# Optimization experiments

Measured on AMD Instinct MI355X. Metric: run time of the kernel, lower is better.

Reference implementation:

```python
import jax, jax.numpy as jnp
import numpy as np

N_NODES = 50000
N_EDGES = 800000
VOCAB = 100000
EMB = 64
HID = 64
N_CLASSES = 10
N_GRAPHS = 512


def setup_inputs() -> dict:
    key = jax.random.key(0)
    ks = jax.random.split(key, 12)
    node_ids = jax.random.randint(ks[0], (N_NODES,), 0, VOCAB)
    edge_index = jax.random.randint(ks[1], (2, N_EDGES), 0, N_NODES)
    batch = jnp.sort(jax.random.randint(ks[2], (N_NODES,), 0, N_GRAPHS))
    emb = jax.random.normal(ks[3], (VOCAB, EMB), jnp.float32)
    s_e = 1.0 / np.sqrt(EMB)
    s_h = 1.0 / np.sqrt(HID)
    Wl0 = jax.random.normal(ks[4], (EMB, HID), jnp.float32) * s_e
    bl0 = jnp.zeros((HID,), jnp.float32)
    Wr0 = jax.random.normal(ks[5], (EMB, HID), jnp.float32) * s_e
    Wl1 = jax.random.normal(ks[6], (HID, HID), jnp.float32) * s_h
    bl1 = jnp.zeros((HID,), jnp.float32)
    Wr1 = jax.random.normal(ks[7], (HID, HID), jnp.float32) * s_h
    Wout = jax.random.normal(ks[8], (HID, N_CLASSES), jnp.float32) * s_h
    bout = jnp.zeros((N_CLASSES,), jnp.float32)
    return {"node_ids": node_ids, "edge_index": edge_index, "batch": batch,
            "emb": emb, "Wl0": Wl0, "bl0": bl0, "Wr0": Wr0,
            "Wl1": Wl1, "bl1": bl1, "Wr1": Wr1, "Wout": Wout, "bout": bout}


def _sage_conv(x, src, dst, Wl, bl, Wr):
    # PyG SAGEConv (aggr='mean'): out_i = lin_l(mean_{j in N(i)} x_j) + lin_r(x_i)
    msg = x[src]                                      # [E, d] gather
    s = jax.ops.segment_sum(msg, dst, num_segments=N_NODES)
    cnt = jax.ops.segment_sum(jnp.ones((msg.shape[0], 1), x.dtype), dst,
                              num_segments=N_NODES)
    mean = jnp.where(cnt > 0, s / jnp.maximum(cnt, 1), 0)
    return mean @ Wl + bl + x @ Wr


def reference(node_ids, edge_index, batch, emb, Wl0, bl0, Wr0, Wl1, bl1, Wr1, Wout, bout):
    x = emb[node_ids]                                  # [N, EMB]
    src, dst = edge_index[0], edge_index[1]
    x = jax.nn.relu(_sage_conv(x, src, dst, Wl0, bl0, Wr0))
    x = jax.nn.relu(_sage_conv(x, src, dst, Wl1, bl1, Wr1))
    # global_mean_pool over graph ids
    s = jax.ops.segment_sum(x, batch, num_segments=N_GRAPHS)
    cnt = jax.ops.segment_sum(jnp.ones((x.shape[0], 1), x.dtype), batch,
                              num_segments=N_GRAPHS)
    pooled = jnp.where(cnt > 0, s / jnp.maximum(cnt, 1), 0)   # [G, HID]
    return pooled @ Wout + bout                        # [G, N_CLASSES]
```

## Files before the change

kernel.cpp:

```cpp
#include <hip/hip_runtime.h>
#include <hip/hip_bf16.h>

#define N_NODES 50000
#define N_EDGES 800000
#define EMB 64
#define HID 64
#define N_CLASSES 10
#define N_GRAPHS 512

#define BKT_SHIFT 6
#define BKT_NODES 64
#define NB_BKT ((N_NODES + BKT_NODES - 1) / BKT_NODES)
#define BKT_CAP 1408
#define CNT_STRIDE 16
#define EB_CHUNK 4096
#define EB_PER_THR (EB_CHUNK / 256)
#define EB_BLOCKS ((N_EDGES + EB_CHUNK - 1) / EB_CHUNK)
#define XFORM_BLOCKS ((N_NODES + 63) / 64)
#define XPAD 68

#define ACC8(vv, A)                                                            \
    do {                                                                       \
        A[0] += __uint_as_float((vv).x << 16);                                 \
        A[1] += __uint_as_float((vv).x & 0xFFFF0000u);                         \
        A[2] += __uint_as_float((vv).y << 16);                                 \
        A[3] += __uint_as_float((vv).y & 0xFFFF0000u);                         \
        A[4] += __uint_as_float((vv).z << 16);                                 \
        A[5] += __uint_as_float((vv).z & 0xFFFF0000u);                         \
        A[6] += __uint_as_float((vv).w << 16);                                 \
        A[7] += __uint_as_float((vv).w & 0xFFFF0000u);                         \
    } while (0)

__device__ __forceinline__ void build_local_csr(
    int bucket, const int* __restrict__ cnt, const int* __restrict__ ebuf,
    unsigned short* lcsr, int* nhist, int* sval, int* sexcl, int* ncur) {
    int tid = threadIdx.x;
    int bs = bucket * BKT_CAP;
    int ne = min(cnt[bucket * CNT_STRIDE], BKT_CAP);
    if (tid < BKT_NODES) { nhist[tid] = 0; ncur[tid] = 0; }
    __syncthreads();
    int held[6];
    int nh = 0;
    for (int i = tid; i < ne; i += 256) held[nh++] = ebuf[bs + i];
#pragma unroll
    for (int j = 0; j < 6; j++)
        if (j < nh) atomicAdd(&nhist[held[j] >> 16], 1);
    __syncthreads();
    if (tid < 64) {
        int v = nhist[tid];
        int s = v;
#pragma unroll
        for (int off = 1; off < 64; off <<= 1) {
            int u = __shfl_up(s, off, 64);
            if (tid >= off) s += u;
        }
        sval[tid] = v;
        sexcl[tid] = s - v;
    }
    __syncthreads();
#pragma unroll
    for (int j = 0; j < 6; j++)
        if (j < nh) {
            int p = held[j];
            int l = p >> 16;
            int r = atomicAdd(&ncur[l], 1);
            lcsr[sexcl[l] + r] = (unsigned short)(p & 0xFFFF);
        }
    __syncthreads();
}

__device__ __forceinline__ void agg2(
    int sA, int dA, int sB, int dB, int sl,
    const unsigned short* lcsr, const __hip_bfloat16* __restrict__ Pb,
    float oA[8], float oB[8]) {
    float a0[8], a1[8], b0[8], b1[8];
#pragma unroll
    for (int j = 0; j < 8; j++) { a0[j] = 0.f; a1[j] = 0.f; b0[j] = 0.f; b1[j] = 0.f; }
    int eA = sA + dA, eB = sB + dB;
    int pA = sA, pB = sB;
    while ((pA + 8 <= eA) && (pB + 8 <= eB)) {
        uint4 vA[8], vB[8];
#pragma unroll
        for (int j = 0; j < 8; j++)
            vA[j] = ((const uint4*)(Pb + (size_t)lcsr[pA + j] * 64))[sl];
#pragma unroll
        for (int j = 0; j < 8; j++)
            vB[j] = ((const uint4*)(Pb + (size_t)lcsr[pB + j] * 64))[sl];
#pragma unroll
        for (int j = 0; j < 8; j++) ACC8(vA[j], ((j & 1) ? a1 : a0));
#pragma unroll
        for (int j = 0; j < 8; j++) ACC8(vB[j], ((j & 1) ? b1 : b0));
        pA += 8; pB += 8;
    }
    while (pA + 8 <= eA) {
        uint4 v[8];
#pragma unroll
        for (int j = 0; j < 8; j++)
            v[j] = ((const uint4*)(Pb + (size_t)lcsr[pA + j] * 64))[sl];
#pragma unroll
        for (int j = 0; j < 8; j++) ACC8(v[j], ((j & 1) ? a1 : a0));
        pA += 8;
    }
    while (pB + 8 <= eB) {
        uint4 v[8];
#pragma unroll
        for (int j = 0; j < 8; j++)
            v[j] = ((const uint4*)(Pb + (size_t)lcsr[pB + j] * 64))[sl];
#pragma unroll
        for (int j = 0; j < 8; j++) ACC8(v[j], ((j & 1) ? b1 : b0));
        pB += 8;
    }
    for (; pA < eA; ++pA) {
        uint4 v = ((const uint4*)(Pb + (size_t)lcsr[pA] * 64))[sl];
        ACC8(v, a0);
    }
    for (; pB < eB; ++pB) {
        uint4 v = ((const uint4*)(Pb + (size_t)lcsr[pB] * 64))[sl];
        ACC8(v, b0);
    }
    float invA = (dA > 0) ? 1.0f / (float)dA : 0.0f;
    float invB = (dB > 0) ? 1.0f / (float)dB : 0.0f;
#pragma unroll
    for (int j = 0; j < 8; j++) {
        oA[j] = (a0[j] + a1[j]) * invA;
        oB[j] = (b0[j] + b1[j]) * invB;
    }
}

__device__ __forceinline__ void finish_row(int node, int sl,
                                           const float* __restrict__ H,
                                           float m[8], float* dst) {
    if (node < N_NODES) {
        size_t off = (size_t)node * 64 + sl * 8;
        float4 q0 = *(const float4*)&H[off];
        float4 q1 = *(const float4*)&H[off + 4];
        m[0] = fmaxf(m[0] + q0.x, 0.f);
        m[1] = fmaxf(m[1] + q0.y, 0.f);
        m[2] = fmaxf(m[2] + q0.z, 0.f);
        m[3] = fmaxf(m[3] + q0.w, 0.f);
        m[4] = fmaxf(m[4] + q1.x, 0.f);
        m[5] = fmaxf(m[5] + q1.y, 0.f);
        m[6] = fmaxf(m[6] + q1.z, 0.f);
        m[7] = fmaxf(m[7] + q1.w, 0.f);
    } else {
#pragma unroll
        for (int j = 0; j < 8; j++) m[j] = 0.f;
    }
    *(float4*)&dst[sl * 8] = make_float4(m[0], m[1], m[2], m[3]);
    *(float4*)&dst[sl * 8 + 4] = make_float4(m[4], m[5], m[6], m[7]);
}

__global__ __launch_bounds__(256) void k_combo(
    const int* __restrict__ esrc, const int* __restrict__ edst,
    int* __restrict__ cnt, int* __restrict__ ebuf,
    const int* __restrict__ ids, const float* __restrict__ emb,
    const float* __restrict__ Wl, const float* __restrict__ bl,
    const float* __restrict__ Wr,
    __hip_bfloat16* __restrict__ Pb, float* __restrict__ Qout) {
    __shared__ float sW[64 * 64];
    __shared__ float sX[64 * XPAD];
    int t = threadIdx.x;
    if (blockIdx.x < EB_BLOCKS) {
        int* h = (int*)sW;
        int* bbase = h + NB_BKT;
        int* cur = (int*)sX;
        for (int i = t; i < NB_BKT; i += 256) { h[i] = 0; cur[i] = 0; }
        __syncthreads();
        int base = blockIdx.x * EB_CHUNK;
        int end = min(base + EB_CHUNK, N_EDGES);
        int dreg[EB_PER_THR];
        int nd = 0;
        for (int i = base + t; i < end; i += 256) dreg[nd++] = edst[i];
#pragma unroll
        for (int j = 0; j < EB_PER_THR; j++)
            if (j < nd) atomicAdd(&h[dreg[j] >> BKT_SHIFT], 1);
        __syncthreads();
        for (int i = t; i < NB_BKT; i += 256)
            if (h[i]) bbase[i] = i * BKT_CAP + atomicAdd(&cnt[i * CNT_STRIDE], h[i]);
        __syncthreads();
        {
            int j = 0;
            for (int i = base + t; i < end; i += 256, j++) {
                int d = dreg[j], s = esrc[i];
                int b = d >> BKT_SHIFT;
                int r = atomicAdd(&cur[b], 1);
                int slot = bbase[b] + r;
                if (slot < (b + 1) * BKT_CAP)
                    ebuf[slot] = ((d & (BKT_NODES - 1)) << 16) | s;
            }
        }
        return;
    }
    int tile = (blockIdx.x - EB_BLOCKS) * 64;
    for (int i = t; i < 64 * 16; i += 256)
        ((float4*)sW)[i] = ((const float4*)Wl)[i];
    for (int i = t; i < 64 * 16; i += 256) {
        int r = i >> 4, c = i & 15;
        int node = tile + r;
        float4 v = make_float4(0.f, 0.f, 0.f, 0.f);
        if (node < N_NODES)
            v = ((const float4*)(emb + (size_t)ids[node] * 64))[c];
        *(float4*)&sX[r * XPAD + c * 4] = v;
    }
    __syncthreads();
    int dg = t & 15, ng = t >> 4;
    float acc[4][4];
#pragma unroll
    for (int i = 0; i < 4; i++)
#pragma unroll
        for (int j = 0; j < 4; j++) acc[i][j] = 0.f;
#pragma unroll 4
    for (int k = 0; k < 64; k++) {
        float4 w = *(const float4*)&sW[k * 64 + dg * 4];
#pragma unroll
        for (int i = 0; i < 4; i++) {
            float xv = sX[(ng + i * 16) * XPAD + k];
            acc[i][0] = fmaf(xv, w.x, acc[i][0]);
            acc[i][1] = fmaf(xv, w.y, acc[i][1]);
            acc[i][2] = fmaf(xv, w.z, acc[i][2]);
            acc[i][3] = fmaf(xv, w.w, acc[i][3]);
        }
    }
#pragma unroll
    for (int i = 0; i < 4; i++) {
        int node = tile + ng + i * 16;
        if (node < N_NODES) {
            union { ushort4 u; __hip_bfloat16 h[4]; } pk;
            pk.h[0] = __float2bfloat16(acc[i][0]);
            pk.h[1] = __float2bfloat16(acc[i][1]);
            pk.h[2] = __float2bfloat16(acc[i][2]);
            pk.h[3] = __float2bfloat16(acc[i][3]);
            *(ushort4*)&Pb[(size_t)node * 64 + dg * 4] = pk.u;
        }
    }
    __syncthreads();
    for (int i = t; i < 64 * 16; i += 256)
        ((float4*)sW)[i] = ((const float4*)Wr)[i];
    __syncthreads();
#pragma unroll
    for (int i = 0; i < 4; i++)
#pragma unroll
        for (int j = 0; j < 4; j++) acc[i][j] = 0.f;
#pragma unroll 4
    for (int k = 0; k < 64; k++) {
        float4 w = *(const float4*)&sW[k * 64 + dg * 4];
#pragma unroll
        for (int i = 0; i < 4; i++) {
            float xv = sX[(ng + i * 16) * XPAD + k];
            acc[i][0] = fmaf(xv, w.x, acc[i][0]);
            acc[i][1] = fmaf(xv, w.y, acc[i][1]);
            acc[i][2] = fmaf(xv, w.z, acc[i][2]);
            acc[i][3] = fmaf(xv, w.w, acc[i][3]);
        }
    }
    float4 blv = *(const float4*)&bl[dg * 4];
#pragma unroll
    for (int i = 0; i < 4; i++) {
        int node = tile + ng + i * 16;
        if (node < N_NODES)
            *(float4*)&Qout[(size_t)node * 64 + dg * 4] =
                make_float4(acc[i][0] + blv.x, acc[i][1] + blv.y,
                            acc[i][2] + blv.z, acc[i][3] + blv.w);
    }
}

__global__ __launch_bounds__(256, 4) void k_fused1(
    const int* __restrict__ cnt, const int* __restrict__ ebuf,
    const __hip_bfloat16* __restrict__ Pb0, const float* __restrict__ Wl,
    const float* __restrict__ bl, const float* __restrict__ Wr,
    __hip_bfloat16* __restrict__ Pb1, float* __restrict__ H) {
    __shared__ float sW[64 * 64];
    __shared__ float sX[64 * XPAD];
    __shared__ unsigned short lcsr[BKT_CAP];
    __shared__ int nhist[BKT_NODES], sval[BKT_NODES], sexcl[BKT_NODES], ncur[BKT_NODES];
    int t = threadIdx.x;
    int tile = blockIdx.x * 64;
    for (int i = t; i < 64 * 16; i += 256)
        ((float4*)sW)[i] = ((const float4*)Wl)[i];
    build_local_csr(blockIdx.x, cnt, ebuf, lcsr, nhist, sval, sexcl, ncur);
    int grp = t >> 3, sl = t & 7;
    int ln0 = grp * 2, ln1 = ln0 + 1;
    float mA[8], mB[8];
    agg2(sexcl[ln0], sval[ln0], sexcl[ln1], sval[ln1], sl, lcsr, Pb0, mA, mB);
    finish_row(tile + ln0, sl, H, mA, &sX[ln0 * XPAD]);
    finish_row(tile + ln1, sl, H, mB, &sX[ln1 * XPAD]);
    __syncthreads();
    int dg = t & 15, ng = t >> 4;
    float acc[4][4];
#pragma unroll
    for (int i = 0; i < 4; i++)
#pragma unroll
        for (int j = 0; j < 4; j++) acc[i][j] = 0.f;
#pragma unroll 4
    for (int k = 0; k < 64; k++) {
        float4 w = *(const float4*)&sW[k * 64 + dg * 4];
#pragma unroll
        for (int i = 0; i < 4; i++) {
            float xv = sX[(ng + i * 16) * XPAD + k];
            acc[i][0] = fmaf(xv, w.x, acc[i][0]);
            acc[i][1] = fmaf(xv, w.y, acc[i][1]);
            acc[i][2] = fmaf(xv, w.z, acc[i][2]);
            acc[i][3] = fmaf(xv, w.w, acc[i][3]);
        }
    }
#pragma unroll
    for (int i = 0; i < 4; i++) {
        int node = tile + ng + i * 16;
        if (node < N_NODES) {
            union { ushort4 u; __hip_bfloat16 h[4]; } pk;
            pk.h[0] = __float2bfloat16(acc[i][0]);
            pk.h[1] = __float2bfloat16(acc[i][1]);
            pk.h[2] = __float2bfloat16(acc[i][2]);
            pk.h[3] = __float2bfloat16(acc[i][3]);
            *(ushort4*)&Pb1[(size_t)node * 64 + dg * 4] = pk.u;
        }
    }
    __syncthreads();
    for (int i = t; i < 64 * 16; i += 256)
        ((float4*)sW)[i] = ((const float4*)Wr)[i];
    __syncthreads();
#pragma unroll
    for (int i = 0; i < 4; i++)
#pragma unroll
        for (int j = 0; j < 4; j++) acc[i][j] = 0.f;
#pragma unroll 4
    for (int k = 0; k < 64; k++) {
        float4 w = *(const float4*)&sW[k * 64 + dg * 4];
#pragma unroll
        for (int i = 0; i < 4; i++) {
            float xv = sX[(ng + i * 16) * XPAD + k];
            acc[i][0] = fmaf(xv, w.x, acc[i][0]);
            acc[i][1] = fmaf(xv, w.y, acc[i][1]);
            acc[i][2] = fmaf(xv, w.z, acc[i][2]);
            acc[i][3] = fmaf(xv, w.w, acc[i][3]);
        }
    }
    float4 blv = *(const float4*)&bl[dg * 4];
#pragma unroll
    for (int i = 0; i < 4; i++) {
        int node = tile + ng + i * 16;
        if (node < N_NODES)
            *(float4*)&H[(size_t)node * 64 + dg * 4] =
                make_float4(acc[i][0] + blv.x, acc[i][1] + blv.y,
                            acc[i][2] + blv.z, acc[i][3] + blv.w);
    }
}

__global__ __launch_bounds__(256, 4) void k_agg2_pool(
    const int* __restrict__ cnt, const int* __restrict__ ebuf,
    const __hip_bfloat16* __restrict__ Pb, const float* __restrict__ H,
    const int* __restrict__ batch, float* __restrict__ psum) {
    __shared__ float sPool[64 * 64];
    __shared__ unsigned short lcsr[BKT_CAP];
    __shared__ int nhist[BKT_NODES], sval[BKT_NODES], sexcl[BKT_NODES], ncur[BKT_NODES];
    __shared__ int sLg[64];
    int t = threadIdx.x;
    int nb = blockIdx.x * 64;
    int gmin = batch[nb];
    if (t < 64) {
        int node = nb + t;
        sLg[t] = batch[node < N_NODES ? node : (N_NODES - 1)] - gmin;
    }
    build_local_csr(blockIdx.x, cnt, ebuf, lcsr, nhist, sval, sexcl, ncur);
    int grp = t >> 3, sl = t & 7;
    int ln0 = grp * 2, ln1 = ln0 + 1;
    float mA[8], mB[8];
    agg2(sexcl[ln0], sval[ln0], sexcl[ln1], sval[ln1], sl, lcsr, Pb, mA, mB);
    finish_row(nb + ln0, sl, H, mA, &sPool[ln0 * 64]);
    finish_row(nb + ln1, sl, H, mB, &sPool[ln1 * 64]);
    __syncthreads();
    int d = t & 63, q = t >> 6;
    int n0 = q * 16;
    float run = 0.f;
    int cur = sLg[n0];
    for (int n = n0; n < n0 + 16; n++) {
        int lg = sLg[n];
        if (lg != cur) {
            if (run != 0.f)
                atomicAdd(&psum[(size_t)(gmin + cur) * 64 + d], run);
            run = 0.f;
            cur = lg;
        }
        run += sPool[n * 64 + d];
    }
    if (run != 0.f)
        atomicAdd(&psum[(size_t)(gmin + cur) * 64 + d], run);
}

__device__ __forceinline__ int lower_bound_batch(const int* __restrict__ batch, int val) {
    int lo = 0, hi = N_NODES;
    while (lo < hi) {
        int mid = (lo + hi) >> 1;
        if (batch[mid] < val) lo = mid + 1; else hi = mid;
    }
    return lo;
}

__global__ __launch_bounds__(256) void k_out(
    const int* __restrict__ batch, const float* __restrict__ psum,
    const float* __restrict__ Wout, const float* __restrict__ bout,
    float* __restrict__ out) {
    int w = threadIdx.x >> 6, lane = threadIdx.x & 63;
    int g = blockIdx.x * 4 + w;
    if (g >= N_GRAPHS) return;
    int s0 = lower_bound_batch(batch, g);
    int s1 = lower_bound_batch(batch, g + 1);
    int cntg = s1 - s0;
    float inv = (cntg > 0) ? 1.0f / (float)cntg : 0.0f;
    float pooled = psum[(size_t)g * 64 + lane] * inv;
#pragma unroll
    for (int c = 0; c < N_CLASSES; c++) {
        float v = pooled * Wout[lane * N_CLASSES + c];
#pragma unroll
        for (int off = 32; off > 0; off >>= 1) v += __shfl_down(v, off, 64);
        if (lane == 0) out[(size_t)g * N_CLASSES + c] = v + bout[c];
    }
}


extern "C" void kernel_launch(void* const* d_in, const int* in_sizes, int n_in,
                              void* d_out, int out_size, void* d_ws, size_t ws_size,
                              hipStream_t stream) {
    const int*   node_ids = (const int*)d_in[0];
    const int*   edge_idx = (const int*)d_in[1];
    const int*   batch    = (const int*)d_in[2];
    const float* emb      = (const float*)d_in[3];
    const float* Wl0      = (const float*)d_in[4];
    const float* bl0      = (const float*)d_in[5];
    const float* Wr0      = (const float*)d_in[6];
    const float* Wl1      = (const float*)d_in[7];
    const float* bl1      = (const float*)d_in[8];
    const float* Wr1      = (const float*)d_in[9];
    const float* Wout     = (const float*)d_in[10];
    const float* bout     = (const float*)d_in[11];
    float* out = (float*)d_out;

    const int* esrc = edge_idx;
    const int* edst = edge_idx + N_EDGES;

    __hip_bfloat16* Pb0 = (__hip_bfloat16*)d_ws;
    __hip_bfloat16* Pb1 = Pb0 + (size_t)N_NODES * 64;
    float* H = (float*)(Pb1 + (size_t)N_NODES * 64);
    int* ebuf = (int*)(H + (size_t)N_NODES * 64);
    int* cnt = ebuf + (size_t)NB_BKT * BKT_CAP;
    float* psum = (float*)(cnt + (size_t)NB_BKT * CNT_STRIDE);

    const int BLK = 256;

    hipMemsetAsync(cnt, 0, (NB_BKT * CNT_STRIDE + N_GRAPHS * 64) * sizeof(int), stream);

    k_combo<<<EB_BLOCKS + XFORM_BLOCKS, BLK, 0, stream>>>(
        esrc, edst, cnt, ebuf, node_ids, emb, Wl0, bl0, Wr0, Pb0, H);

    k_fused1<<<XFORM_BLOCKS, BLK, 0, stream>>>(cnt, ebuf, Pb0, Wl1, bl1, Wr1, Pb1, H);

    k_agg2_pool<<<NB_BKT, BLK, 0, stream>>>(cnt, ebuf, Pb1, H, batch, psum);

    k_out<<<(N_GRAPHS + 3) / 4, BLK, 0, stream>>>(batch, psum, Wout, bout, out);
}
```

Before: 188.3 us.

## Pad CSR segments to a zero row, software-pipeline gathers, fuse dual GEMM

Pads each node's local CSR segment to a multiple of 8 entries, filling the padding with a dedicated all-zero sentinel row in the bf16 feature tables. This lets the aggregation loop issue fixed groups of 4 gathers, double-buffered across iterations, with no scalar tail loops. The two per-tile GEMMs (lin_l and lin_r) are merged into one pass that reads weights directly from global or L1 instead of staging them in shared memory. This frees LDS and removes barriers, but adds wasted gathers of the zero row and more accumulator registers.

Result: faster. 183.7 us (-2.5%).

```diff
diff --git a/kernel.cpp b/kernel.cpp
--- a/kernel.cpp
+++ b/kernel.cpp
@@ -18,6 +18,9 @@
 #define EB_BLOCKS ((N_EDGES + EB_CHUNK - 1) / EB_CHUNK)
 #define XFORM_BLOCKS ((N_NODES + 63) / 64)
 #define XPAD 68
+#define ZROW N_NODES
+#define LCSR_SZ 1856
+#define LCSR_FULL 1864
 
 #define ACC8(vv, A)                                                            \
     do {                                                                       \
@@ -38,6 +41,7 @@
     int bs = bucket * BKT_CAP;
     int ne = min(cnt[bucket * CNT_STRIDE], BKT_CAP);
     if (tid < BKT_NODES) { nhist[tid] = 0; ncur[tid] = 0; }
+    for (int i = tid; i < LCSR_FULL; i += 256) lcsr[i] = (unsigned short)ZROW;
     __syncthreads();
     int held[6];
     int nh = 0;
@@ -48,14 +52,15 @@
     __syncthreads();
     if (tid < 64) {
         int v = nhist[tid];
-        int s = v;
+        int p = (v + 7) & ~7;
+        int s = p;
 #pragma unroll
         for (int off = 1; off < 64; off <<= 1) {
             int u = __shfl_up(s, off, 64);
             if (tid >= off) s += u;
         }
         sval[tid] = v;
-        sexcl[tid] = s - v;
+        sexcl[tid] = s - p;
     }
     __syncthreads();
 #pragma unroll
@@ -76,47 +81,43 @@
     float a0[8], a1[8], b0[8], b1[8];
 #pragma unroll
     for (int j = 0; j < 8; j++) { a0[j] = 0.f; a1[j] = 0.f; b0[j] = 0.f; b1[j] = 0.f; }
-    int eA = sA + dA, eB = sB + dB;
-    int pA = sA, pB = sB;
-    while ((pA + 8 <= eA) && (pB + 8 <= eB)) {
-        uint4 vA[8], vB[8];
-#pragma unroll
-        for (int j = 0; j < 8; j++)
-            vA[j] = ((const uint4*)(Pb + (size_t)lcsr[pA + j] * 64))[sl];
-#pragma unroll
-        for (int j = 0; j < 8; j++)
-            vB[j] = ((const uint4*)(Pb + (size_t)lcsr[pB + j] * 64))[sl];
-#pragma unroll
-        for (int j = 0; j < 8; j++) ACC8(vA[j], ((j & 1) ? a1 : a0));
-#pragma unroll
-        for (int j = 0; j < 8; j++) ACC8(vB[j], ((j & 1) ? b1 : b0));
-        pA += 8; pB += 8;
-    }
-    while (pA + 8 <= eA) {
-        uint4 v[8];
-#pragma unroll
-        for (int j = 0; j < 8; j++)
-            v[j] = ((const uint4*)(Pb + (size_t)lcsr[pA + j] * 64))[sl];
-#pragma unroll
-        for (int j = 0; j < 8; j++) ACC8(v[j], ((j & 1) ? a1 : a0));
-        pA += 8;
-    }
-    while (pB + 8 <= eB) {
-        uint4 v[8];
-#pragma unroll
-        for (int j = 0; j < 8; j++)
-            v[j] = ((const uint4*)(Pb + (size_t)lcsr[pB + j] * 64))[sl];
-#pragma unroll
-        for (int j = 0; j < 8; j++) ACC8(v[j], ((j & 1) ? b1 : b0));
-        pB += 8;
-    }
-    for (; pA < eA; ++pA) {
-        uint4 v = ((const uint4*)(Pb + (size_t)lcsr[pA] * 64))[sl];
-        ACC8(v, a0);
-    }
-    for (; pB < eB; ++pB) {
-        uint4 v = ((const uint4*)(Pb + (size_t)lcsr[pB] * 64))[sl];
-        ACC8(v, b0);
+    int nA = (dA + 3) >> 2, nB = (dB + 3) >> 2;
+    int n = max(nA, nB);
+    int mA = max(nA - 1, 0), mB = max(nB - 1, 0);
+    if (n > 0) {
+        uint4 A0[4], A1[4], B0[4], B1[4];
+#define LD4(D, base_)                                                          \
+        {                                                                      \
+            int _p = (base_);                                                  \
+            D[0] = ((const uint4*)(Pb + (size_t)lcsr[_p + 0] * 64))[sl];       \
+            D[1] = ((const uint4*)(Pb + (size_t)lcsr[_p + 1] * 64))[sl];       \
+            D[2] = ((const uint4*)(Pb + (size_t)lcsr[_p + 2] * 64))[sl];       \
+            D[3] = ((const uint4*)(Pb + (size_t)lcsr[_p + 3] * 64))[sl];       \
+        }
+#define AC4(S, X0, X1)                                                         \
+        { ACC8(S[0], X0); ACC8(S[1], X1); ACC8(S[2], X0); ACC8(S[3], X1); }
+        LD4(A0, sA); LD4(B0, sB);
+        int c = 1;
+        for (; c + 1 < n; c += 2) {
+            LD4(A1, sA + 4 * min(c, mA)); LD4(B1, sB + 4 * min(c, mB));
+            if (c - 1 < nA) AC4(A0, a0, a1);
+            if (c - 1 < nB) AC4(B0, b0, b1);
+            LD4(A0, sA + 4 * min(c + 1, mA)); LD4(B0, sB + 4 * min(c + 1, mB));
+            if (c < nA) AC4(A1, a0, a1);
+            if (c < nB) AC4(B1, b0, b1);
+        }
+        if (c < n) {
+            LD4(A1, sA + 4 * min(c, mA)); LD4(B1, sB + 4 * min(c, mB));
+            if (c - 1 < nA) AC4(A0, a0, a1);
+            if (c - 1 < nB) AC4(B0, b0, b1);
+            if (c < nA) AC4(A1, a0, a1);
+            if (c < nB) AC4(B1, b0, b1);
+        } else {
+            if (c - 1 < nA) AC4(A0, a0, a1);
+            if (c - 1 < nB) AC4(B0, b0, b1);
+        }
+#undef LD4
+#undef AC4
     }
     float invA = (dA > 0) ? 1.0f / (float)dA : 0.0f;
     float invB = (dB > 0) ? 1.0f / (float)dB : 0.0f;
@@ -150,20 +151,71 @@
     *(float4*)&dst[sl * 8 + 4] = make_float4(m[4], m[5], m[6], m[7]);
 }
 
+__device__ __forceinline__ void gemm_dual_from_sX(
+    int tile, int t, const float* sX,
+    const float* __restrict__ Wl, const float* __restrict__ Wr,
+    const float* __restrict__ bl,
+    __hip_bfloat16* __restrict__ Pb, float* __restrict__ Qout) {
+    int dg = t & 15, ng = t >> 4;
+    float accL[4][4], accR[4][4];
+#pragma unroll
+    for (int i = 0; i < 4; i++)
+#pragma unroll
+        for (int j = 0; j < 4; j++) { accL[i][j] = 0.f; accR[i][j] = 0.f; }
+#pragma unroll 4
+    for (int k = 0; k < 64; k++) {
+        float4 wl = ((const float4*)Wl)[k * 16 + dg];
+        float4 wr = ((const float4*)Wr)[k * 16 + dg];
+#pragma unroll
+        for (int i = 0; i < 4; i++) {
+            float xv = sX[(ng + i * 16) * XPAD + k];
+            accL[i][0] = fmaf(xv, wl.x, accL[i][0]);
+            accL[i][1] = fmaf(xv, wl.y, accL[i][1]);
+            accL[i][2] = fmaf(xv, wl.z, accL[i][2]);
+            accL[i][3] = fmaf(xv, wl.w, accL[i][3]);
+            accR[i][0] = fmaf(xv, wr.x, accR[i][0]);
+            accR[i][1] = fmaf(xv, wr.y, accR[i][1]);
+            accR[i][2] = fmaf(xv, wr.z, accR[i][2]);
+            accR[i][3] = fmaf(xv, wr.w, accR[i][3]);
+        }
+    }
+    float4 blv = ((const float4*)bl)[dg];
+#pragma unroll
+    for (int i = 0; i < 4; i++) {
+        int node = tile + ng + i * 16;
+        if (node < N_NODES) {
+            union { ushort4 u; __hip_bfloat16 h[4]; } pk;
+            pk.h[0] = __float2bfloat16(accL[i][0]);
+            pk.h[1] = __float2bfloat16(accL[i][1]);
+            pk.h[2] = __float2bfloat16(accL[i][2]);
+            pk.h[3] = __float2bfloat16(accL[i][3]);
+            *(ushort4*)&Pb[(size_t)node * 64 + dg * 4] = pk.u;
+            *(float4*)&Qout[(size_t)node * 64 + dg * 4] =
+                make_float4(accR[i][0] + blv.x, accR[i][1] + blv.y,
+                            accR[i][2] + blv.z, accR[i][3] + blv.w);
+        }
+    }
+}
+
 __global__ __launch_bounds__(256) void k_combo(
     const int* __restrict__ esrc, const int* __restrict__ edst,
     int* __restrict__ cnt, int* __restrict__ ebuf,
     const int* __restrict__ ids, const float* __restrict__ emb,
     const float* __restrict__ Wl, const float* __restrict__ bl,
     const float* __restrict__ Wr,
-    __hip_bfloat16* __restrict__ Pb, float* __restrict__ Qout) {
-    __shared__ float sW[64 * 64];
+    __hip_bfloat16* __restrict__ Pb, __hip_bfloat16* __restrict__ Pb1z,
+    float* __restrict__ Qout) {
     __shared__ float sX[64 * XPAD];
     int t = threadIdx.x;
     if (blockIdx.x < EB_BLOCKS) {
-        int* h = (int*)sW;
+        if (blockIdx.x == 0 && t < 16) {
+            uint4 z = make_uint4(0u, 0u, 0u, 0u);
+            if (t < 8) ((uint4*)(Pb + (size_t)ZROW * 64))[t] = z;
+            else       ((uint4*)(Pb1z + (size_t)ZROW * 64))[t - 8] = z;
+        }
+        int* h = (int*)sX;
         int* bbase = h + NB_BKT;
-        int* cur = (int*)sX;
+        int* cur = bbase + NB_BKT;
         for (int i = t; i < NB_BKT; i += 256) { h[i] = 0; cur[i] = 0; }
         __syncthreads();
         int base = blockIdx.x * EB_CHUNK;
@@ -192,8 +244,6 @@
         return;
     }
     int tile = (blockIdx.x - EB_BLOCKS) * 64;
-    for (int i = t; i < 64 * 16; i += 256)
-        ((float4*)sW)[i] = ((const float4*)Wl)[i];
     for (int i = t; i < 64 * 16; i += 256) {
         int r = i >> 4, c = i & 15;
         int node = tile + r;
@@ -203,65 +253,7 @@
         *(float4*)&sX[r * XPAD + c * 4] = v;
     }
     __syncthreads();
-    int dg = t & 15, ng = t >> 4;
-    float acc[4][4];
-#pragma unroll
-    for (int i = 0; i < 4; i++)
-#pragma unroll
-        for (int j = 0; j < 4; j++) acc[i][j] = 0.f;
-#pragma unroll 4
-    for (int k = 0; k < 64; k++) {
-        float4 w = *(const float4*)&sW[k * 64 + dg * 4];
-#pragma unroll
-        for (int i = 0; i < 4; i++) {
-            float xv = sX[(ng + i * 16) * XPAD + k];
-            acc[i][0] = fmaf(xv, w.x, acc[i][0]);
-            acc[i][1] = fmaf(xv, w.y, acc[i][1]);
-            acc[i][2] = fmaf(xv, w.z, acc[i][2]);
-            acc[i][3] = fmaf(xv, w.w, acc[i][3]);
-        }
-    }
-#pragma unroll
-    for (int i = 0; i < 4; i++) {
-        int node = tile + ng + i * 16;
-        if (node < N_NODES) {
-            union { ushort4 u; __hip_bfloat16 h[4]; } pk;
-            pk.h[0] = __float2bfloat16(acc[i][0]);
-            pk.h[1] = __float2bfloat16(acc[i][1]);
-            pk.h[2] = __float2bfloat16(acc[i][2]);
-            pk.h[3] = __float2bfloat16(acc[i][3]);
-            *(ushort4*)&Pb[(size_t)node * 64 + dg * 4] = pk.u;
-        }
-    }
-    __syncthreads();
-    for (int i = t; i < 64 * 16; i += 256)
-        ((float4*)sW)[i] = ((const float4*)Wr)[i];
-    __syncthreads();
-#pragma unroll
-    for (int i = 0; i < 4; i++)
-#pragma unroll
-        for (int j = 0; j < 4; j++) acc[i][j] = 0.f;
-#pragma unroll 4
-    for (int k = 0; k < 64; k++) {
-        float4 w = *(const float4*)&sW[k * 64 + dg * 4];
-#pragma unroll
-        for (int i = 0; i < 4; i++) {
-            float xv = sX[(ng + i * 16) * XPAD + k];
-            acc[i][0] = fmaf(xv, w.x, acc[i][0]);
-            acc[i][1] = fmaf(xv, w.y, acc[i][1]);
-            acc[i][2] = fmaf(xv, w.z, acc[i][2]);
-            acc[i][3] = fmaf(xv, w.w, acc[i][3]);
-        }
-    }
-    float4 blv = *(const float4*)&bl[dg * 4];
-#pragma unroll
-    for (int i = 0; i < 4; i++) {
-        int node = tile + ng + i * 16;
-        if (node < N_NODES)
-            *(float4*)&Qout[(size_t)node * 64 + dg * 4] =
-                make_float4(acc[i][0] + blv.x, acc[i][1] + blv.y,
-                            acc[i][2] + blv.z, acc[i][3] + blv.w);
-    }
+    gemm_dual_from_sX(tile, t, sX, Wl, Wr, bl, Pb, Qout);
 }
 
 __global__ __launch_bounds__(256, 4) void k_fused1(
@@ -269,14 +261,11 @@
     const __hip_bfloat16* __restrict__ Pb0, const float* __restrict__ Wl,
     const float* __restrict__ bl, const float* __restrict__ Wr,
     __hip_bfloat16* __restrict__ Pb1, float* __restrict__ H) {
-    __shared__ float sW[64 * 64];
     __shared__ float sX[64 * XPAD];
-    __shared__ unsigned short lcsr[BKT_CAP];
+    __shared__ unsigned short lcsr[LCSR_FULL];
     __shared__ int nhist[BKT_NODES], sval[BKT_NODES], sexcl[BKT_NODES], ncur[BKT_NODES];
     int t = threadIdx.x;
     int tile = blockIdx.x * 64;
-    for (int i = t; i < 64 * 16; i += 256)
-        ((float4*)sW)[i] = ((const float4*)Wl)[i];
     build_local_csr(blockIdx.x, cnt, ebuf, lcsr, nhist, sval, sexcl, ncur);
     int grp = t >> 3, sl = t & 7;
     int ln0 = grp * 2, ln1 = ln0 + 1;
@@ -285,65 +274,7 @@
     finish_row(tile + ln0, sl, H, mA, &sX[ln0 * XPAD]);
     finish_row(tile + ln1, sl, H, mB, &sX[ln1 * XPAD]);
     __syncthreads();
-    int dg = t & 15, ng = t >> 4;
-    float acc[4][4];
-#pragma unroll
-    for (int i = 0; i < 4; i++)
-#pragma unroll
-        for (int j = 0; j < 4; j++) acc[i][j] = 0.f;
-#pragma unroll 4
-    for (int k = 0; k < 64; k++) {
-        float4 w = *(const float4*)&sW[k * 64 + dg * 4];
-#pragma unroll
-        for (int i = 0; i < 4; i++) {
-            float xv = sX[(ng + i * 16) * XPAD + k];
-            acc[i][0] = fmaf(xv, w.x, acc[i][0]);
-            acc[i][1] = fmaf(xv, w.y, acc[i][1]);
-            acc[i][2] = fmaf(xv, w.z, acc[i][2]);
-            acc[i][3] = fmaf(xv, w.w, acc[i][3]);
-        }
-    }
-#pragma unroll
-    for (int i = 0; i < 4; i++) {
-        int node = tile + ng + i * 16;
-        if (node < N_NODES) {
-            union { ushort4 u; __hip_bfloat16 h[4]; } pk;
-            pk.h[0] = __float2bfloat16(acc[i][0]);
-            pk.h[1] = __float2bfloat16(acc[i][1]);
-            pk.h[2] = __float2bfloat16(acc[i][2]);
-            pk.h[3] = __float2bfloat16(acc[i][3]);
-            *(ushort4*)&Pb1[(size_t)node * 64 + dg * 4] = pk.u;
-        }
-    }
-    __syncthreads();
-    for (int i = t; i < 64 * 16; i += 256)
-        ((float4*)sW)[i] = ((const float4*)Wr)[i];
-    __syncthreads();
-#pragma unroll
-    for (int i = 0; i < 4; i++)
-#pragma unroll
-        for (int j = 0; j < 4; j++) acc[i][j] = 0.f;
-#pragma unroll 4
-    for (int k = 0; k < 64; k++) {
-        float4 w = *(const float4*)&sW[k * 64 + dg * 4];
-#pragma unroll
-        for (int i = 0; i < 4; i++) {
-            float xv = sX[(ng + i * 16) * XPAD + k];
-            acc[i][0] = fmaf(xv, w.x, acc[i][0]);
-            acc[i][1] = fmaf(xv, w.y, acc[i][1]);
-            acc[i][2] = fmaf(xv, w.z, acc[i][2]);
-            acc[i][3] = fmaf(xv, w.w, acc[i][3]);
-        }
-    }
-    float4 blv = *(const float4*)&bl[dg * 4];
-#pragma unroll
-    for (int i = 0; i < 4; i++) {
-        int node = tile + ng + i * 16;
-        if (node < N_NODES)
-            *(float4*)&H[(size_t)node * 64 + dg * 4] =
-                make_float4(acc[i][0] + blv.x, acc[i][1] + blv.y,
-                            acc[i][2] + blv.z, acc[i][3] + blv.w);
-    }
+    gemm_dual_from_sX(tile, t, sX, Wl, Wr, bl, Pb1, H);
 }
 
 __global__ __launch_bounds__(256, 4) void k_agg2_pool(
@@ -351,7 +282,7 @@
     const __hip_bfloat16* __restrict__ Pb, const float* __restrict__ H,
     const int* __restrict__ batch, float* __restrict__ psum) {
     __shared__ float sPool[64 * 64];
-    __shared__ unsigned short lcsr[BKT_CAP];
+    __shared__ unsigned short lcsr[LCSR_FULL];
     __shared__ int nhist[BKT_NODES], sval[BKT_NODES], sexcl[BKT_NODES], ncur[BKT_NODES];
     __shared__ int sLg[64];
     int t = threadIdx.x;
@@ -439,8 +370,8 @@
     const int* edst = edge_idx + N_EDGES;
 
     __hip_bfloat16* Pb0 = (__hip_bfloat16*)d_ws;
-    __hip_bfloat16* Pb1 = Pb0 + (size_t)N_NODES * 64;
-    float* H = (float*)(Pb1 + (size_t)N_NODES * 64);
+    __hip_bfloat16* Pb1 = Pb0 + (size_t)(N_NODES + 1) * 64;
+    float* H = (float*)(Pb1 + (size_t)(N_NODES + 1) * 64);
     int* ebuf = (int*)(H + (size_t)N_NODES * 64);
     int* cnt = ebuf + (size_t)NB_BKT * BKT_CAP;
     float* psum = (float*)(cnt + (size_t)NB_BKT * CNT_STRIDE);
@@ -450,7 +381,7 @@
     hipMemsetAsync(cnt, 0, (NB_BKT * CNT_STRIDE + N_GRAPHS * 64) * sizeof(int), stream);
 
     k_combo<<<EB_BLOCKS + XFORM_BLOCKS, BLK, 0, stream>>>(
-        esrc, edst, cnt, ebuf, node_ids, emb, Wl0, bl0, Wr0, Pb0, H);
+        esrc, edst, cnt, ebuf, node_ids, emb, Wl0, bl0, Wr0, Pb0, Pb1, H);
 
     k_fused1<<<XFORM_BLOCKS, BLK, 0, stream>>>(cnt, ebuf, Pb0, Wl1, bl1, Wr1, Pb1, H);
 
```
